# Kernel optimization log

Hardware: AMD Instinct MI355X
Metric: run time of the kernel (lower is better)

The kernel has to match this reference:

```python
import jax, jax.numpy as jnp
import numpy as np

B, N, K, H, NHEADS = 2, 2000, 32, 128, 4
EPS = 1e-6


def setup_inputs() -> dict:
    key = jax.random.key(0)
    ks = jax.random.split(key, 16)
    h_V = jax.random.normal(ks[0], (B, N, H), jnp.float32)
    h_EV = jax.random.normal(ks[1], (B, N, K, 2 * H), jnp.float32)
    h_KV = jax.random.normal(ks[2], (B, N, K, H), jnp.float32)
    h_KE = jax.random.normal(ks[3], (B, N, K, H), jnp.float32)
    mask_V = jax.random.randint(ks[4], (B, N), 0, 2).astype(jnp.float32)
    mask_attend = jax.random.randint(ks[5], (B, N, K), 0, 2).astype(jnp.float32)
    # guarantee at least one valid neighbor per node so masked softmax is finite
    mask_attend = mask_attend.at[:, :, 0].set(1.0)
    s = 1.0 / np.sqrt(H)
    W_Q = jax.random.normal(ks[6], (H, H), jnp.float32) * s
    W_K1 = jax.random.normal(ks[7], (H, H), jnp.float32) * s
    W_K2 = jax.random.normal(ks[8], (H, H), jnp.float32) * s
    W_V = jax.random.normal(ks[9], (H, 2 * H), jnp.float32) * s
    W_O = jax.random.normal(ks[10], (H, H), jnp.float32) * s
    gain = jnp.ones((H,), jnp.float32)
    bias = jnp.zeros((H,), jnp.float32)
    return dict(h_V=h_V, h_EV=h_EV, h_KV=h_KV, h_KE=h_KE, mask_V=mask_V,
                mask_attend=mask_attend, W_Q=W_Q, W_K1=W_K1, W_K2=W_K2,
                W_V=W_V, W_O=W_O, gain=gain, bias=bias)


def reference(h_V, h_EV, h_KV, h_KE, mask_V, mask_attend,
              W_Q, W_K1, W_K2, W_V, W_O, gain, bias):
    d = H // NHEADS  # per-head dim
    # Linear layers (torch Linear: x @ W.T), split heads
    Q = (h_V @ W_Q.T).reshape(B, N, 1, NHEADS, d)        # [B,N,1,h,d]
    K1 = (h_KE @ W_K1.T).reshape(B, N, K, NHEADS, d)     # [B,N,K,h,d]
    K2 = (h_KV @ W_K2.T).reshape(B, N, K, NHEADS, d)
    V = (h_EV @ W_V.T).reshape(B, N, K, NHEADS, d)
    # QKK: elementwise triple product reduced over d -> [B,N,K,h] -> [B,N,h,K]
    logits = jnp.sum(Q * K1 * K2, axis=-1)
    logits = jnp.swapaxes(logits, -2, -1) / d            # [B,N,h,K]
    # masked softmax over neighbors
    mask = jnp.broadcast_to(mask_attend[:, :, None, :], logits.shape)
    neg_inf = jnp.float32(np.finfo(np.float32).min)
    attend = jax.nn.softmax(jnp.where(mask > 0, logits, neg_inf), axis=-1)
    attend = mask * attend
    # aggregate neighbors per head, merge heads, output projection
    h_up = jnp.einsum('bnhk,bnkhd->bnhd', attend, V).reshape(B, N, H)
    dh = h_up @ W_O.T
    # residual + Normalize (torch .var is unbiased -> ddof=1)
    x = h_V + dh
    mu = x.mean(-1, keepdims=True)
    sigma = jnp.sqrt(x.var(-1, ddof=1, keepdims=True) + EPS)
    out = gain * (x - mu) / (sigma + EPS) + bias
    return mask_V[..., None] * out
```

## Files before the change

### kernel.cpp

```cpp
#include <hip/hip_runtime.h>
#include <hip/hip_bf16.h>
#include <math.h>

#define BN_TOTAL 4000
#define NODES 4
#define KN 32
#define HD 128
#define NH 4

typedef unsigned short ushort_t;
typedef unsigned int u32;
typedef short bf16x8 __attribute__((ext_vector_type(8)));
typedef float f32x4  __attribute__((ext_vector_type(4)));

__device__ __forceinline__ float bf2f(ushort_t u) {
    return __uint_as_float(((u32)u) << 16);
}
__device__ __forceinline__ ushort_t f2bf(float f) {
    u32 u = __float_as_uint(f);
    u += 0x7FFFu + ((u >> 16) & 1u);
    return (ushort_t)(u >> 16);
}
__device__ __forceinline__ u32 pack2bf(float lo, float hi) {
    return ((u32)f2bf(hi) << 16) | (u32)f2bf(lo);
}
__device__ __forceinline__ void cvt8(uint4 w, float* f) {
    f[0] = __uint_as_float(w.x << 16); f[1] = __uint_as_float(w.x & 0xFFFF0000u);
    f[2] = __uint_as_float(w.y << 16); f[3] = __uint_as_float(w.y & 0xFFFF0000u);
    f[4] = __uint_as_float(w.z << 16); f[5] = __uint_as_float(w.z & 0xFFFF0000u);
    f[6] = __uint_as_float(w.w << 16); f[7] = __uint_as_float(w.w & 0xFFFF0000u);
}

template<bool ISBF>
__device__ __forceinline__ void load8(const void* base, int idx, float* f) {
    if (ISBF) {
        uint4 v = *reinterpret_cast<const uint4*>((const ushort_t*)base + idx);
        cvt8(v, f);
    } else {
        const float* p = (const float*)base + idx;
        float4 a = *reinterpret_cast<const float4*>(p);
        float4 b = *reinterpret_cast<const float4*>(p + 4);
        f[0] = a.x; f[1] = a.y; f[2] = a.z; f[3] = a.w;
        f[4] = b.x; f[5] = b.y; f[6] = b.z; f[7] = b.w;
    }
}
template<bool ISBF>
__device__ __forceinline__ float load1(const void* base, int idx) {
    return ISBF ? bf2f(((const ushort_t*)base)[idx]) : ((const float*)base)[idx];
}
template<bool ISBF>
__device__ __forceinline__ bf16x8 loadfrag(const void* base, int idx) {
    if (ISBF) {
        return *reinterpret_cast<const bf16x8*>((const ushort_t*)base + idx);
    } else {
        const float* p = (const float*)base + idx;
        float4 a = *reinterpret_cast<const float4*>(p);
        float4 b = *reinterpret_cast<const float4*>(p + 4);
        bf16x8 r;
        r[0] = (short)f2bf(a.x); r[1] = (short)f2bf(a.y);
        r[2] = (short)f2bf(a.z); r[3] = (short)f2bf(a.w);
        r[4] = (short)f2bf(b.x); r[5] = (short)f2bf(b.y);
        r[6] = (short)f2bf(b.z); r[7] = (short)f2bf(b.w);
        return r;
    }
}

template<bool ISBF>
__device__ __forceinline__ void stage_chunk(const void* W, int elem_off, u32* sW,
                                            int chunk, int lane) {
    if (ISBF) {
        uint4 v = *reinterpret_cast<const uint4*>((const ushort_t*)W + elem_off);
        *reinterpret_cast<uint4*>(sW + chunk * 256 + lane * 4) = v;
    } else {
        const float* p = (const float*)W + elem_off;
        float4 a = *reinterpret_cast<const float4*>(p);
        float4 b = *reinterpret_cast<const float4*>(p + 4);
        uint4 v;
        v.x = pack2bf(a.x, a.y); v.y = pack2bf(a.z, a.w);
        v.z = pack2bf(b.x, b.y); v.w = pack2bf(b.z, b.w);
        *reinterpret_cast<uint4*>(sW + chunk * 256 + lane * 4) = v;
    }
}
__device__ __forceinline__ bf16x8 read_frag(const u32* sW, int chunk, int lane) {
    return *reinterpret_cast<const bf16x8*>(
        reinterpret_cast<const ushort_t*>(sW) + chunk * 512 + lane * 8);
}

template<bool ISBF>
__device__ __forceinline__ void run4(
    const void* h_V, const void* h_EV, const void* h_KV, const void* h_KE,
    const void* mask_V, const void* mask_att,
    const void* W_Q, const void* W_K1, const void* W_K2,
    const void* W_Vw, const void* W_O, const void* gain, const void* bias,
    void* out,
    u32* sW, float* shV, float* sQ, float* sLog, float* sAtt, float* sHU)
{
    const int t    = threadIdx.x;
    const int w    = t >> 6;
    const int lane = t & 63;
    const int quad = lane >> 4;
    const int lr   = lane & 15;
    const int node = blockIdx.x * NODES + w;
    const int c1   = lane, c2 = lane + 64;

    const float mA1 = load1<ISBF>(mask_att, node * KN + lr);
    const float mA2 = load1<ISBF>(mask_att, node * KN + 16 + lr);
    const float mV  = load1<ISBF>(mask_V, node);
    const float gn1 = load1<ISBF>(gain, c1), gn2 = load1<ISBF>(gain, c2);
    const float bs1 = load1<ISBF>(bias, c1), bs2 = load1<ISBF>(bias, c2);

    #pragma unroll
    for (int j = 0; j < 16; ++j) {
        const int c  = w * 16 + j;
        const int ks = (c >> 3) & 3, nt = c & 7;
        const void* W = (c < 32) ? W_K1 : W_K2;
        stage_chunk<ISBF>(W, (nt * 16 + lr) * HD + ks * 32 + quad * 8, sW, c, lane);
    }

    shV[w * HD + 2 * lane]     = load1<ISBF>(h_V, node * HD + 2 * lane);
    shV[w * HD + 2 * lane + 1] = load1<ISBF>(h_V, node * HD + 2 * lane + 1);

    bf16x8 aKE[2][4], aKV[2][4];
    const int aoff = node * KN * HD;
    #pragma unroll
    for (int mt = 0; mt < 2; ++mt)
        #pragma unroll
        for (int ks = 0; ks < 4; ++ks) {
            const int eo = aoff + (mt * 16 + lr) * HD + ks * 32 + quad * 8;
            aKE[mt][ks] = loadfrag<ISBF>(h_KE, eo);
            aKV[mt][ks] = loadfrag<ISBF>(h_KV, eo);
        }
    __syncthreads();

    {
        float q1 = 0.f, q2 = 0.f;
        #pragma unroll 4
        for (int jc = 0; jc < HD; jc += 8) {
            float hv[8];
            #pragma unroll
            for (int j = 0; j < 8; ++j) hv[j] = shV[w * HD + jc + j];
            float w1[8], w2[8];
            load8<ISBF>(W_Q, c1 * HD + jc, w1);
            load8<ISBF>(W_Q, c2 * HD + jc, w2);
            #pragma unroll
            for (int j = 0; j < 8; ++j) { q1 += w1[j] * hv[j]; q2 += w2[j] * hv[j]; }
        }
        sQ[w * HD + c1] = q1;
        sQ[w * HD + c2] = q2;
    }
    __syncthreads();

    float qv[8];
    #pragma unroll
    for (int nt = 0; nt < 8; ++nt) qv[nt] = sQ[w * HD + nt * 16 + lr];

    const f32x4 zero4 = {0.f, 0.f, 0.f, 0.f};
    #pragma unroll
    for (int h = 0; h < NH; ++h) {
        f32x4 a1[2][2], a2[2][2];
        #pragma unroll
        for (int mt = 0; mt < 2; ++mt)
            #pragma unroll
            for (int j = 0; j < 2; ++j) { a1[mt][j] = zero4; a2[mt][j] = zero4; }
        #pragma unroll
        for (int ks = 0; ks < 4; ++ks) {
            #pragma unroll
            for (int j = 0; j < 2; ++j) {
                const int nt = 2 * h + j;
                bf16x8 b1 = read_frag(sW, ks * 8 + nt, lane);
                bf16x8 b2 = read_frag(sW, 32 + ks * 8 + nt, lane);
                #pragma unroll
                for (int mt = 0; mt < 2; ++mt) {
                    a1[mt][j] = __builtin_amdgcn_mfma_f32_16x16x32_bf16(aKE[mt][ks], b1, a1[mt][j], 0, 0, 0);
                    a2[mt][j] = __builtin_amdgcn_mfma_f32_16x16x32_bf16(aKV[mt][ks], b2, a2[mt][j], 0, 0, 0);
                }
            }
        }
        #pragma unroll
        for (int mt = 0; mt < 2; ++mt) {
            #pragma unroll
            for (int r = 0; r < 4; ++r) {
                float p = qv[2 * h] * a1[mt][0][r] * a2[mt][0][r]
                        + qv[2 * h + 1] * a1[mt][1][r] * a2[mt][1][r];
                p += __shfl_xor(p, 1); p += __shfl_xor(p, 2);
                p += __shfl_xor(p, 4); p += __shfl_xor(p, 8);
                if (lr == 0)
                    sLog[w * HD + h * KN + mt * 16 + quad * 4 + r] = p * (1.f / 32.f);
            }
        }
    }
    __syncthreads();

    #pragma unroll
    for (int j = 0; j < 16; ++j) {
        const int c  = w * 16 + j;
        const int ks = c >> 3, nt = c & 7;
        stage_chunk<ISBF>(W_Vw, (nt * 16 + lr) * 256 + ks * 32 + quad * 8, sW, c, lane);
    }
    bf16x8 aEV[2][8];
    const int eoff = node * KN * 256;
    #pragma unroll
    for (int mt = 0; mt < 2; ++mt)
        #pragma unroll
        for (int ks = 0; ks < 8; ++ks)
            aEV[mt][ks] = loadfrag<ISBF>(h_EV, eoff + (mt * 16 + lr) * 256 + ks * 32 + quad * 8);

    {
        const int h = quad;
        float l1 = sLog[w * HD + h * KN + lr];
        float l2 = sLog[w * HD + h * KN + 16 + lr];
        const float NEG = -3.402823466e38f;
        l1 = (mA1 > 0.f) ? l1 : NEG;
        l2 = (mA2 > 0.f) ? l2 : NEG;
        float mx = fmaxf(l1, l2);
        #pragma unroll
        for (int d = 1; d < 16; d <<= 1) mx = fmaxf(mx, __shfl_xor(mx, d));
        float e1 = __expf(l1 - mx), e2 = __expf(l2 - mx);
        float ss = e1 + e2;
        #pragma unroll
        for (int d = 1; d < 16; d <<= 1) ss += __shfl_xor(ss, d);
        float inv = 1.f / ss;
        sAtt[w * HD + h * KN + lr]      = mA1 * e1 * inv;
        sAtt[w * HD + h * KN + 16 + lr] = mA2 * e2 * inv;
    }
    __syncthreads();

    #pragma unroll
    for (int h = 0; h < NH; ++h) {
        f32x4 cv[2][2];
        #pragma unroll
        for (int mt = 0; mt < 2; ++mt)
            #pragma unroll
            for (int j = 0; j < 2; ++j) cv[mt][j] = zero4;
        #pragma unroll
        for (int ks = 0; ks < 8; ++ks) {
            #pragma unroll
            for (int j = 0; j < 2; ++j) {
                bf16x8 b = read_frag(sW, ks * 8 + 2 * h + j, lane);
                #pragma unroll
                for (int mt = 0; mt < 2; ++mt)
                    cv[mt][j] = __builtin_amdgcn_mfma_f32_16x16x32_bf16(aEV[mt][ks], b, cv[mt][j], 0, 0, 0);
            }
        }
        float hu0 = 0.f, hu1 = 0.f;
        #pragma unroll
        for (int mt = 0; mt < 2; ++mt) {
            #pragma unroll
            for (int r = 0; r < 4; ++r) {
                float a = sAtt[w * HD + h * KN + mt * 16 + quad * 4 + r];
                hu0 += a * cv[mt][0][r];
                hu1 += a * cv[mt][1][r];
            }
        }
        hu0 += __shfl_xor(hu0, 16); hu0 += __shfl_xor(hu0, 32);
        hu1 += __shfl_xor(hu1, 16); hu1 += __shfl_xor(hu1, 32);
        if (quad == 0) {
            sHU[w * HD + (2 * h) * 16 + lr]     = hu0;
            sHU[w * HD + (2 * h + 1) * 16 + lr] = hu1;
        }
    }
    __syncthreads();

    {
        float d1 = 0.f, d2 = 0.f;
        #pragma unroll 4
        for (int jc = 0; jc < HD; jc += 8) {
            float hv[8];
            #pragma unroll
            for (int j = 0; j < 8; ++j) hv[j] = sHU[w * HD + jc + j];
            float w1[8], w2[8];
            load8<ISBF>(W_O, c1 * HD + jc, w1);
            load8<ISBF>(W_O, c2 * HD + jc, w2);
            #pragma unroll
            for (int j = 0; j < 8; ++j) { d1 += w1[j] * hv[j]; d2 += w2[j] * hv[j]; }
        }
        float x1 = shV[w * HD + c1] + d1;
        float x2 = shV[w * HD + c2] + d2;
        float s  = x1 + x2;
        float s2 = x1 * x1 + x2 * x2;
        #pragma unroll
        for (int d = 1; d < 64; d <<= 1) {
            s  += __shfl_xor(s, d);
            s2 += __shfl_xor(s2, d);
        }
        float mu    = s * (1.f / 128.f);
        float var   = (s2 - 128.f * mu * mu) * (1.f / 127.f);
        float sigma = sqrtf(var + 1e-6f);
        float inv   = 1.f / (sigma + 1e-6f);
        float o1 = mV * (gn1 * (x1 - mu) * inv + bs1);
        float o2 = mV * (gn2 * (x2 - mu) * inv + bs2);
        if (ISBF) {
            ((ushort_t*)out)[node * HD + c1] = f2bf(o1);
            ((ushort_t*)out)[node * HD + c2] = f2bf(o2);
        } else {
            ((float*)out)[node * HD + c1] = o1;
            ((float*)out)[node * HD + c2] = o2;
        }
    }
}

__global__ __launch_bounds__(256, 2) void spatppi_kernel(
    const void* h_V, const void* h_EV, const void* h_KV, const void* h_KE,
    const void* mask_V, const void* mask_att,
    const void* W_Q, const void* W_K1, const void* W_K2,
    const void* W_Vw, const void* W_O, const void* gain, const void* bias,
    void* out)
{
    __shared__ u32 sW[16384];
    __shared__ float shV[NODES * HD];
    __shared__ float sQ[NODES * HD];
    __shared__ float sLog[NODES * HD];
    __shared__ float sAtt[NODES * HD];
    __shared__ float sHU[NODES * HD];

    const bool isbf = (((const u32*)gain)[0] != 0x3F800000u);
    if (isbf)
        run4<true >(h_V, h_EV, h_KV, h_KE, mask_V, mask_att, W_Q, W_K1, W_K2,
                    W_Vw, W_O, gain, bias, out, sW, shV, sQ, sLog, sAtt, sHU);
    else
        run4<false>(h_V, h_EV, h_KV, h_KE, mask_V, mask_att, W_Q, W_K1, W_K2,
                    W_Vw, W_O, gain, bias, out, sW, shV, sQ, sLog, sAtt, sHU);
}

extern "C" void kernel_launch(void* const* d_in, const int* in_sizes, int n_in,
                              void* d_out, int out_size, void* d_ws, size_t ws_size,
                              hipStream_t stream) {
    spatppi_kernel<<<dim3(BN_TOTAL / NODES), dim3(256), 0, stream>>>(
        d_in[0], d_in[1], d_in[2], d_in[3], d_in[4], d_in[5],
        d_in[6], d_in[7], d_in[8], d_in[9], d_in[10], d_in[11], d_in[12],
        d_out);
}
```

Baseline: 352.1 us.

## Process eight nodes per block and stage K and V weights concurrently

Doubles the block to 512 threads with eight nodes, so weight staging to LDS is amortized over twice as many nodes. W_K1/W_K2 and W_V are staged up front into separate LDS buffers, and h_EV fragments are loaded together with h_KE/h_KV, which removes the mid-kernel restaging and most block barriers. Q is shared by wave shuffles instead of going through LDS. The cost is more LDS per block (about 144KB), which may limit occupancy, and much higher register pressure from holding all A fragments at once.

Result: slower. 400.0 us (+13.6%).

```diff
diff --git a/kernel.cpp b/kernel.cpp
--- a/kernel.cpp
+++ b/kernel.cpp
@@ -3,7 +3,7 @@
 #include <math.h>
 
 #define BN_TOTAL 4000
-#define NODES 4
+#define NODES 8
 #define KN 32
 #define HD 128
 #define NH 4
@@ -87,13 +87,13 @@
 }
 
 template<bool ISBF>
-__device__ __forceinline__ void run4(
+__device__ __forceinline__ void run8(
     const void* h_V, const void* h_EV, const void* h_KV, const void* h_KE,
     const void* mask_V, const void* mask_att,
     const void* W_Q, const void* W_K1, const void* W_K2,
     const void* W_Vw, const void* W_O, const void* gain, const void* bias,
     void* out,
-    u32* sW, float* shV, float* sQ, float* sLog, float* sAtt, float* sHU)
+    u32* sWK, u32* sWV, float* sBuf)
 {
     const int t    = threadIdx.x;
     const int w    = t >> 6;
@@ -103,6 +103,11 @@
     const int node = blockIdx.x * NODES + w;
     const int c1   = lane, c2 = lane + 64;
 
+    float* shV  = sBuf + w * 512;
+    float* sLog = shV + 128;
+    float* sAtt = shV + 256;
+    float* sHU  = shV + 384;
+
     const float mA1 = load1<ISBF>(mask_att, node * KN + lr);
     const float mA2 = load1<ISBF>(mask_att, node * KN + 16 + lr);
     const float mV  = load1<ISBF>(mask_V, node);
@@ -110,49 +115,61 @@
     const float bs1 = load1<ISBF>(bias, c1), bs2 = load1<ISBF>(bias, c2);
 
     #pragma unroll
-    for (int j = 0; j < 16; ++j) {
-        const int c  = w * 16 + j;
+    for (int j = 0; j < 8; ++j) {
+        const int c  = w * 8 + j;
         const int ks = (c >> 3) & 3, nt = c & 7;
         const void* W = (c < 32) ? W_K1 : W_K2;
-        stage_chunk<ISBF>(W, (nt * 16 + lr) * HD + ks * 32 + quad * 8, sW, c, lane);
-    }
-
-    shV[w * HD + 2 * lane]     = load1<ISBF>(h_V, node * HD + 2 * lane);
-    shV[w * HD + 2 * lane + 1] = load1<ISBF>(h_V, node * HD + 2 * lane + 1);
-
-    bf16x8 aKE[2][4], aKV[2][4];
-    const int aoff = node * KN * HD;
+        stage_chunk<ISBF>(W, (nt * 16 + lr) * HD + ks * 32 + quad * 8, sWK, c, lane);
+    }
     #pragma unroll
-    for (int mt = 0; mt < 2; ++mt)
-        #pragma unroll
-        for (int ks = 0; ks < 4; ++ks) {
-            const int eo = aoff + (mt * 16 + lr) * HD + ks * 32 + quad * 8;
-            aKE[mt][ks] = loadfrag<ISBF>(h_KE, eo);
-            aKV[mt][ks] = loadfrag<ISBF>(h_KV, eo);
-        }
+    for (int j = 0; j < 8; ++j) {
+        const int c  = w * 8 + j;
+        const int ks = c >> 3, nt = c & 7;
+        stage_chunk<ISBF>(W_Vw, (nt * 16 + lr) * 256 + ks * 32 + quad * 8, sWV, c, lane);
+    }
+
+    shV[2 * lane]     = load1<ISBF>(h_V, node * HD + 2 * lane);
+    shV[2 * lane + 1] = load1<ISBF>(h_V, node * HD + 2 * lane + 1);
+
+    bf16x8 aKE[2][4], aKV[2][4], aEV[2][8];
+    {
+        const int aoff = node * KN * HD;
+        #pragma unroll
+        for (int mt = 0; mt < 2; ++mt)
+            #pragma unroll
+            for (int ks = 0; ks < 4; ++ks) {
+                const int eo = aoff + (mt * 16 + lr) * HD + ks * 32 + quad * 8;
+                aKE[mt][ks] = loadfrag<ISBF>(h_KE, eo);
+                aKV[mt][ks] = loadfrag<ISBF>(h_KV, eo);
+            }
+        const int eoff = node * KN * 256;
+        #pragma unroll
+        for (int mt = 0; mt < 2; ++mt)
+            #pragma unroll
+            for (int ks = 0; ks < 8; ++ks)
+                aEV[mt][ks] = loadfrag<ISBF>(h_EV, eoff + (mt * 16 + lr) * 256 + ks * 32 + quad * 8);
+    }
     __syncthreads();
 
+    float qv[8];
     {
         float q1 = 0.f, q2 = 0.f;
         #pragma unroll 4
         for (int jc = 0; jc < HD; jc += 8) {
             float hv[8];
             #pragma unroll
-            for (int j = 0; j < 8; ++j) hv[j] = shV[w * HD + jc + j];
+            for (int j = 0; j < 8; ++j) hv[j] = shV[jc + j];
             float w1[8], w2[8];
             load8<ISBF>(W_Q, c1 * HD + jc, w1);
             load8<ISBF>(W_Q, c2 * HD + jc, w2);
             #pragma unroll
             for (int j = 0; j < 8; ++j) { q1 += w1[j] * hv[j]; q2 += w2[j] * hv[j]; }
         }
-        sQ[w * HD + c1] = q1;
-        sQ[w * HD + c2] = q2;
-    }
-    __syncthreads();
-
-    float qv[8];
-    #pragma unroll
-    for (int nt = 0; nt < 8; ++nt) qv[nt] = sQ[w * HD + nt * 16 + lr];
+        #pragma unroll
+        for (int nt = 0; nt < 4; ++nt) qv[nt] = __shfl(q1, nt * 16 + lr);
+        #pragma unroll
+        for (int nt = 4; nt < 8; ++nt) qv[nt] = __shfl(q2, (nt - 4) * 16 + lr);
+    }
 
     const f32x4 zero4 = {0.f, 0.f, 0.f, 0.f};
     #pragma unroll
@@ -167,8 +184,8 @@
             #pragma unroll
             for (int j = 0; j < 2; ++j) {
                 const int nt = 2 * h + j;
-                bf16x8 b1 = read_frag(sW, ks * 8 + nt, lane);
-                bf16x8 b2 = read_frag(sW, 32 + ks * 8 + nt, lane);
+                bf16x8 b1 = read_frag(sWK, ks * 8 + nt, lane);
+                bf16x8 b2 = read_frag(sWK, 32 + ks * 8 + nt, lane);
                 #pragma unroll
                 for (int mt = 0; mt < 2; ++mt) {
                     a1[mt][j] = __builtin_amdgcn_mfma_f32_16x16x32_bf16(aKE[mt][ks], b1, a1[mt][j], 0, 0, 0);
@@ -185,30 +202,15 @@
                 p += __shfl_xor(p, 1); p += __shfl_xor(p, 2);
                 p += __shfl_xor(p, 4); p += __shfl_xor(p, 8);
                 if (lr == 0)
-                    sLog[w * HD + h * KN + mt * 16 + quad * 4 + r] = p * (1.f / 32.f);
-            }
-        }
-    }
-    __syncthreads();
-
-    #pragma unroll
-    for (int j = 0; j < 16; ++j) {
-        const int c  = w * 16 + j;
-        const int ks = c >> 3, nt = c & 7;
-        stage_chunk<ISBF>(W_Vw, (nt * 16 + lr) * 256 + ks * 32 + quad * 8, sW, c, lane);
-    }
-    bf16x8 aEV[2][8];
-    const int eoff = node * KN * 256;
-    #pragma unroll
-    for (int mt = 0; mt < 2; ++mt)
-        #pragma unroll
-        for (int ks = 0; ks < 8; ++ks)
-            aEV[mt][ks] = loadfrag<ISBF>(h_EV, eoff + (mt * 16 + lr) * 256 + ks * 32 + quad * 8);
+                    sLog[h * KN + mt * 16 + quad * 4 + r] = p * (1.f / 32.f);
+            }
+        }
+    }
 
     {
         const int h = quad;
-        float l1 = sLog[w * HD + h * KN + lr];
-        float l2 = sLog[w * HD + h * KN + 16 + lr];
+        float l1 = sLog[h * KN + lr];
+        float l2 = sLog[h * KN + 16 + lr];
         const float NEG = -3.402823466e38f;
         l1 = (mA1 > 0.f) ? l1 : NEG;
         l2 = (mA2 > 0.f) ? l2 : NEG;
@@ -220,10 +222,9 @@
         #pragma unroll
         for (int d = 1; d < 16; d <<= 1) ss += __shfl_xor(ss, d);
         float inv = 1.f / ss;
-        sAtt[w * HD + h * KN + lr]      = mA1 * e1 * inv;
-        sAtt[w * HD + h * KN + 16 + lr] = mA2 * e2 * inv;
-    }
-    __syncthreads();
+        sAtt[h * KN + lr]      = mA1 * e1 * inv;
+        sAtt[h * KN + 16 + lr] = mA2 * e2 * inv;
+    }
 
     #pragma unroll
     for (int h = 0; h < NH; ++h) {
@@ -236,7 +237,7 @@
         for (int ks = 0; ks < 8; ++ks) {
             #pragma unroll
             for (int j = 0; j < 2; ++j) {
-                bf16x8 b = read_frag(sW, ks * 8 + 2 * h + j, lane);
+                bf16x8 b = read_frag(sWV, ks * 8 + 2 * h + j, lane);
                 #pragma unroll
                 for (int mt = 0; mt < 2; ++mt)
                     cv[mt][j] = __builtin_amdgcn_mfma_f32_16x16x32_bf16(aEV[mt][ks], b, cv[mt][j], 0, 0, 0);
@@ -247,7 +248,7 @@
         for (int mt = 0; mt < 2; ++mt) {
             #pragma unroll
             for (int r = 0; r < 4; ++r) {
-                float a = sAtt[w * HD + h * KN + mt * 16 + quad * 4 + r];
+                float a = sAtt[h * KN + mt * 16 + quad * 4 + r];
                 hu0 += a * cv[mt][0][r];
                 hu1 += a * cv[mt][1][r];
             }
@@ -255,11 +256,10 @@
         hu0 += __shfl_xor(hu0, 16); hu0 += __shfl_xor(hu0, 32);
         hu1 += __shfl_xor(hu1, 16); hu1 += __shfl_xor(hu1, 32);
         if (quad == 0) {
-            sHU[w * HD + (2 * h) * 16 + lr]     = hu0;
-            sHU[w * HD + (2 * h + 1) * 16 + lr] = hu1;
-        }
-    }
-    __syncthreads();
+            sHU[(2 * h) * 16 + lr]     = hu0;
+            sHU[(2 * h + 1) * 16 + lr] = hu1;
+        }
+    }
 
     {
         float d1 = 0.f, d2 = 0.f;
@@ -267,15 +267,15 @@
         for (int jc = 0; jc < HD; jc += 8) {
             float hv[8];
             #pragma unroll
-            for (int j = 0; j < 8; ++j) hv[j] = sHU[w * HD + jc + j];
+            for (int j = 0; j < 8; ++j) hv[j] = sHU[jc + j];
             float w1[8], w2[8];
             load8<ISBF>(W_O, c1 * HD + jc, w1);
             load8<ISBF>(W_O, c2 * HD + jc, w2);
             #pragma unroll
             for (int j = 0; j < 8; ++j) { d1 += w1[j] * hv[j]; d2 += w2[j] * hv[j]; }
         }
-        float x1 = shV[w * HD + c1] + d1;
-        float x2 = shV[w * HD + c2] + d2;
+        float x1 = shV[c1] + d1;
+        float x2 = shV[c2] + d2;
         float s  = x1 + x2;
         float s2 = x1 * x1 + x2 * x2;
         #pragma unroll
@@ -299,33 +299,30 @@
     }
 }
 
-__global__ __launch_bounds__(256, 2) void spatppi_kernel(
+__global__ __launch_bounds__(512, 2) void spatppi_kernel(
     const void* h_V, const void* h_EV, const void* h_KV, const void* h_KE,
     const void* mask_V, const void* mask_att,
     const void* W_Q, const void* W_K1, const void* W_K2,
     const void* W_Vw, const void* W_O, const void* gain, const void* bias,
     void* out)
 {
-    __shared__ u32 sW[16384];
-    __shared__ float shV[NODES * HD];
-    __shared__ float sQ[NODES * HD];
-    __shared__ float sLog[NODES * HD];
-    __shared__ float sAtt[NODES * HD];
-    __shared__ float sHU[NODES * HD];
+    __shared__ u32 sWK[16384];
+    __shared__ u32 sWV[16384];
+    __shared__ float sBuf[NODES * 512];
 
     const bool isbf = (((const u32*)gain)[0] != 0x3F800000u);
     if (isbf)
-        run4<true >(h_V, h_EV, h_KV, h_KE, mask_V, mask_att, W_Q, W_K1, W_K2,
-                    W_Vw, W_O, gain, bias, out, sW, shV, sQ, sLog, sAtt, sHU);
+        run8<true >(h_V, h_EV, h_KV, h_KE, mask_V, mask_att, W_Q, W_K1, W_K2,
+                    W_Vw, W_O, gain, bias, out, sWK, sWV, sBuf);
     else
-        run4<false>(h_V, h_EV, h_KV, h_KE, mask_V, mask_att, W_Q, W_K1, W_K2,
-                    W_Vw, W_O, gain, bias, out, sW, shV, sQ, sLog, sAtt, sHU);
+        run8<false>(h_V, h_EV, h_KV, h_KE, mask_V, mask_att, W_Q, W_K1, W_K2,
+                    W_Vw, W_O, gain, bias, out, sWK, sWV, sBuf);
 }
 
 extern "C" void kernel_launch(void* const* d_in, const int* in_sizes, int n_in,
                               void* d_out, int out_size, void* d_ws, size_t ws_size,
                               hipStream_t stream) {
-    spatppi_kernel<<<dim3(BN_TOTAL / NODES), dim3(256), 0, stream>>>(
+    spatppi_kernel<<<dim3(BN_TOTAL / NODES), dim3(512), 0, stream>>>(
         d_in[0], d_in[1], d_in[2], d_in[3], d_in[4], d_in[5],
         d_in[6], d_in[7], d_in[8], d_in[9], d_in[10], d_in[11], d_in[12],
         d_out);
```
